# Kernel tuning notes

Measured on AMD Instinct MI355X. Metric: run time of the kernel, lower is better.

## Reference

```python
import jax, jax.numpy as jnp
import numpy as np

DIM = 64
PATCH = 8
KH = KW = 7
K = KH * KW
PAD = 3


def conv2d(x, w, pad):
    return jax.lax.conv_general_dilated(
        x, w, window_strides=(1, 1), padding=[(pad, pad), (pad, pad)],
        dimension_numbers=('NCHW', 'OIHW', 'NCHW'))


def deform_conv2d(x, offset, mask, weight):
    # torchvision modulated deformable conv v2, stride=1, dilation=1, pad=PAD
    B, C, H, W = x.shape
    off = offset.reshape(B, K, 2, H, W)  # channel pairs are (dy, dx)
    ky, kx = jnp.meshgrid(jnp.arange(KH), jnp.arange(KW), indexing='ij')
    ky = ky.reshape(K).astype(x.dtype)
    kx = kx.reshape(K).astype(x.dtype)
    hh = jnp.arange(H, dtype=x.dtype)
    ww = jnp.arange(W, dtype=x.dtype)
    # sampling locations: p0 - pad + p_k + offset, shape [B,K,H,W]
    y = hh[None, None, :, None] - PAD + ky[None, :, None, None] + off[:, :, 0]
    xx = ww[None, None, None, :] - PAD + kx[None, :, None, None] + off[:, :, 1]

    y0 = jnp.floor(y)
    x0 = jnp.floor(xx)
    wy = y - y0
    wx = xx - x0

    img_flat = x.reshape(B, C, H * W)

    def gather(yi, xi):
        valid = (yi >= 0) & (yi < H) & (xi >= 0) & (xi < W)
        yc = jnp.clip(yi, 0, H - 1).astype(jnp.int32)
        xc = jnp.clip(xi, 0, W - 1).astype(jnp.int32)
        lin = (yc * W + xc).reshape(B, -1)  # [B, K*H*W]
        v = jax.vmap(lambda im, idx: im[:, idx])(img_flat, lin)  # [B,C,K*H*W]
        v = v.reshape(B, C, K, H, W)
        return v * valid[:, None].astype(x.dtype)

    val = ((1 - wy) * (1 - wx))[:, None] * gather(y0, x0) \
        + ((1 - wy) * wx)[:, None] * gather(y0, x0 + 1) \
        + (wy * (1 - wx))[:, None] * gather(y0 + 1, x0) \
        + (wy * wx)[:, None] * gather(y0 + 1, x0 + 1)
    val = val * mask[:, None]  # modulation, [B,C,K,H,W]
    wf = weight.reshape(weight.shape[0], weight.shape[1], K)
    return jnp.einsum('bckhw,ock->bohw', val, wf)


def setup_inputs() -> dict:
    key = jax.random.key(0)
    ks = jax.random.split(key, 12)
    B, C, H, W = 1, DIM, 192, 192
    s = 0.05
    return {
        'enc': jax.random.normal(ks[0], (B, C, H, W), jnp.float32),
        'dec': jax.random.normal(ks[1], (B, C, H, W), jnp.float32),
        'inverse_offset': jax.random.normal(ks[2], (B, 2 * K, H, W), jnp.float32),
        'inverse_weight': jax.random.uniform(ks[3], (B, K, H, W), jnp.float32),
        'w_proj_in': jax.random.normal(ks[4], (C, C, 1, 1), jnp.float32) * s,
        'fft_w': 1.0 + 0.1 * jax.random.normal(ks[5], (C, 1, 1, PATCH, PATCH // 2 + 1), jnp.float32),
        'w_proj_out': jax.random.normal(ks[6], (2 * C, 2 * C, 1, 1), jnp.float32) * s,
        'w_deform': jax.random.normal(ks[7], (C, C, KH, KW), jnp.float32) * s,
        'w_conv1': jax.random.normal(ks[8], (C, C, 1, 1), jnp.float32) * s,
        'w_conv2': jax.random.normal(ks[9], (C, C, 3, 3), jnp.float32) * s,
    }


def reference(enc, dec, inverse_offset, inverse_weight, w_proj_in, fft_w,
              w_proj_out, w_deform, w_conv1, w_conv2):
    B, C, h, w = enc.shape
    reverse = deform_conv2d(enc, inverse_offset, inverse_weight, w_deform)
    reverse = conv2d(reverse, w_conv1, 0)

    e = conv2d(enc, w_proj_in, 0)
    # check_image_size: pad H,W to multiples of PATCH (no-op for 192)
    ph = (-h) % PATCH
    pw = (-w) % PATCH
    e = jnp.pad(e, ((0, 0), (0, 0), (0, ph), (0, pw)))
    Hp, Wp = h + ph, w + pw
    # [B,C,h',w',p1,p2]
    xp = e.reshape(B, C, Hp // PATCH, PATCH, Wp // PATCH, PATCH).transpose(0, 1, 2, 4, 3, 5)
    xf = jnp.fft.rfft2(xp.astype(jnp.float32)) * fft_w  # fft_w [C,1,1,8,5] broadcasts
    xp = jnp.fft.irfft2(xf, s=(PATCH, PATCH))
    e = xp.transpose(0, 1, 2, 4, 3, 5).reshape(B, C, Hp, Wp)[:, :, :h, :w]

    e = e + reverse
    e = conv2d(e, w_conv2, 1)
    feat = jnp.concatenate([e, dec], axis=1)
    feat = conv2d(feat, w_proj_out, 0)
    x1, x2 = jnp.split(feat, 2, axis=1)  # SimpleGate
    return x1 * x2
```

## Files before the change

kernel.cpp:

```cpp
#include <hip/hip_runtime.h>
#include <math.h>

#define CH    64
#define WW    192
#define HH    192
#define HWSZ  (192*192)
#define KK    49
#define ROWP  68
#define SROW  72
#define C3ROW 72
#define OROW  136

typedef __attribute__((ext_vector_type(8))) short     s16x8;
typedef __attribute__((ext_vector_type(8))) _Float16  h16x8;
typedef __attribute__((ext_vector_type(2))) _Float16  h16x2;
typedef __attribute__((ext_vector_type(2))) __fp16    fp16x2;
typedef __attribute__((ext_vector_type(4))) float     f32x4;

__device__ __forceinline__ unsigned short f2h(float f) {
    union { _Float16 h; unsigned short s; } u; u.h = (_Float16)f;
    return u.s;
}

__device__ __forceinline__ unsigned pkh(float lo, float hi) {
    union { fp16x2 h; unsigned u; } v;
    v.h = __builtin_amdgcn_cvt_pkrtz(lo, hi);
    return v.u;
}

__device__ __forceinline__ h16x2 cvt2h(float a) {
    union { fp16x2 h; h16x2 o; } v;
    v.h = __builtin_amdgcn_cvt_pkrtz(a, a);
    return v.o;
}

__device__ __forceinline__ h16x2 as_h2(unsigned u) {
    union { unsigned u; h16x2 h; } v; v.u = u; return v.h;
}

__device__ __forceinline__ unsigned as_u(h16x2 h) {
    union { h16x2 h; unsigned u; } v; v.h = h; return v.u;
}

__device__ const float c_cos8[8] = {
    1.f, 0.70710678118654752f, 0.f, -0.70710678118654752f,
   -1.f, -0.70710678118654752f, 0.f, 0.70710678118654752f };

__global__ __launch_bounds__(256) void k_prep(
    const float* __restrict__ fw,
    const float* __restrict__ wd,
    const float* __restrict__ w2,
    const float* __restrict__ wc1,
    const float* __restrict__ wpo,
    const float* __restrict__ wpi,
    float* __restrict__ krT,
    short* __restrict__ wA,
    short* __restrict__ w2A,
    short* __restrict__ wpoA,
    short* __restrict__ wpiA)
{
    int tid = blockIdx.x * blockDim.x + threadIdx.x;
    int nt  = gridDim.x * blockDim.x;
    for (int t = tid; t < 64 * 64; t += nt) {
        int uv = t >> 6, c = t & 63;
        int u = uv >> 3, v = uv & 7;
        float acc = 0.f;
        for (int ky = 0; ky < 8; ky++)
            for (int kx = 0; kx < 8; kx++) {
                float wv = (kx <= 4) ? fw[c * 40 + ky * 5 + kx]
                                     : fw[c * 40 + ((8 - ky) & 7) * 5 + (8 - kx)];
                acc += wv * c_cos8[(ky * u + kx * v) & 7];
            }
        krT[uv * 64 + c] = acc * (1.f / 64.f);
    }
    for (int t = tid; t < 9 * 4096; t += nt) {
        int tap = t / 4096, rem = t & 4095;
        int o = rem >> 6, c = rem & 63;
        float v = w2[(o * 64 + c) * 9 + tap];
        int fi = tap * 8 + (o >> 4) * 2 + (c >> 5);
        int ln = ((c >> 3) & 3) * 16 + (o & 15);
        w2A[fi * 512 + ln * 8 + (c & 7)] = (short)f2h(v);
    }
    for (int t = tid; t < 128 * 128; t += nt) {
        int o = t >> 7, c = t & 127;
        int fi = (o >> 4) * 4 + (c >> 5);
        int ln = ((c >> 3) & 3) * 16 + (o & 15);
        wpoA[fi * 512 + ln * 8 + (c & 7)] = (short)f2h(wpo[t]);
    }
    for (int t = tid; t < 64 * 64; t += nt) {
        int o = t >> 6, c = t & 63;
        int fi = (o >> 4) * 2 + (c >> 5);
        int ln = ((c >> 3) & 3) * 16 + (o & 15);
        wpiA[fi * 512 + ln * 8 + (c & 7)] = (short)f2h(wpi[t]);
    }

    __shared__ float wdk [64 * ROWP];
    __shared__ float wc1s[64 * ROWP];
    int k = blockIdx.x;
    int t = threadIdx.x;
#pragma unroll
    for (int r = 0; r < 16; r++) {
        int idx = t + r * 256;
        int o = idx >> 6, c = idx & 63;
        wdk [o * ROWP + c] = wd[(o * 64 + c) * KK + k];
        wc1s[o * ROWP + c] = wc1[o * 64 + c];
    }
    __syncthreads();

    int ot = (t >> 4) * 4, cb = (t & 15) * 4;
    float a[4][4];
#pragma unroll
    for (int i = 0; i < 4; i++)
#pragma unroll
        for (int j = 0; j < 4; j++) a[i][j] = 0.f;
    for (int o = 0; o < 64; o++) {
        float wv_[4], sv_[4];
#pragma unroll
        for (int i = 0; i < 4; i++) wv_[i] = wc1s[(ot + i) * ROWP + o];
#pragma unroll
        for (int j = 0; j < 4; j++) sv_[j] = wdk[o * ROWP + cb + j];
#pragma unroll
        for (int i = 0; i < 4; i++)
#pragma unroll
            for (int j = 0; j < 4; j++) a[i][j] += wv_[i] * sv_[j];
    }
#pragma unroll
    for (int i = 0; i < 4; i++)
#pragma unroll
        for (int j = 0; j < 4; j++) {
            int o2 = ot + i, c = cb + j;
            int tt = o2 >> 4, m = o2 & 15;
            int kt = c >> 5, q = (c >> 3) & 3, jj = c & 7;
            int ln = q * 16 + m;
            wA[(k * 8 + tt * 2 + kt) * 512 + ln * 8 + jj] = (short)f2h(a[i][j]);
        }
}

__global__ __launch_bounds__(256) void k_trans(
    const float* __restrict__ enc, unsigned short* __restrict__ encH)
{
    __shared__ float s[64 * 65];
    int t = threadIdx.x;
    int base = blockIdx.x * 64;
#pragma unroll
    for (int r = 0; r < 16; r++) {
        int idx = t + r * 256;
        int p = idx & 63, c = idx >> 6;
        s[p * 65 + c] = enc[c * HWSZ + base + p];
    }
    __syncthreads();
#pragma unroll
    for (int r = 0; r < 8; r++) {
        int idx = t + r * 256;
        int pr = idx & 31, p = idx >> 5;
        ((unsigned*)encH)[(base + p) * 32 + pr] =
            pkh(s[p * 65 + 2 * pr], s[p * 65 + 2 * pr + 1]);
    }
}

#define REDW 20

__global__ __launch_bounds__(256) void k_deform(
    const unsigned short* __restrict__ encH, const float* __restrict__ off,
    const float* __restrict__ msk, const short* __restrict__ wA,
    float* __restrict__ rev)
{
    __shared__ __align__(16) short sm[4][16 * SROW];
    __shared__ __align__(16) float red[2 * 64 * REDW];

    int t = threadIdx.x;
    int lane = t & 63, w = t >> 6;
    int b = blockIdx.x;
    int xcd = b & 7, blk = b >> 3;
    int gy  = xcd * 24 + blk / 12;
    int gx0 = (blk % 12) * 16;

    int sp = lane >> 2, g = lane & 3;
    int sgx  = gx0 + sp;
    int gp_s = gy * WW + sgx;
    int n = lane & 15, q = lane >> 4;
    short* smw = &sm[w][0];

    f32x4 acc[4];
#pragma unroll
    for (int ot = 0; ot < 4; ot++) acc[ot] = (f32x4){0.f, 0.f, 0.f, 0.f};

    int kstart = (w == 0) ? 0 : 13 + (w - 1) * 12;
    int kend   = (w == 0) ? 13 : kstart + 12;

    float dy = off[(2 * kstart) * HWSZ + gp_s];
    float dx = off[(2 * kstart + 1) * HWSZ + gp_s];
    float mm = msk[kstart * HWSZ + gp_s];

#pragma unroll 1
    for (int k = kstart; k < kend; k++) {
        int ky = k / 7, kx = k % 7;
        float y = (float)(gy  - 3 + ky) + dy;
        float x = (float)(sgx - 3 + kx) + dx;
        float y0f = floorf(y), x0f = floorf(x);
        float wy = y - y0f, wx = x - x0f;
        int iy0 = (int)y0f, ix0 = (int)x0f;
        int iy1 = iy0 + 1, ix1 = ix0 + 1;
        bool vy0 = (iy0 >= 0) & (iy0 < HH);
        bool vy1 = (iy1 >= 0) & (iy1 < HH);
        bool vx0 = (ix0 >= 0) & (ix0 < WW);
        bool vx1 = (ix1 >= 0) & (ix1 < WW);
        int iy0c = min(max(iy0, 0), HH - 1), iy1c = min(max(iy1, 0), HH - 1);
        int ix0c = min(max(ix0, 0), WW - 1), ix1c = min(max(ix1, 0), WW - 1);
        float a00 = (vy0 & vx0) ? (1.f - wy) * (1.f - wx) * mm : 0.f;
        float a01 = (vy0 & vx1) ? (1.f - wy) * wx * mm : 0.f;
        float a10 = (vy1 & vx0) ? wy * (1.f - wx) * mm : 0.f;
        float a11 = (vy1 & vx1) ? wy * wx * mm : 0.f;

        const unsigned short* b00p = encH + (iy0c * WW + ix0c) * 64 + g * 16;
        const unsigned short* b01p = encH + (iy0c * WW + ix1c) * 64 + g * 16;
        const unsigned short* b10p = encH + (iy1c * WW + ix0c) * 64 + g * 16;
        const unsigned short* b11p = encH + (iy1c * WW + ix1c) * 64 + g * 16;
        uint4 u00[2], u01[2], u10[2], u11[2];
        u00[0] = *(const uint4*)b00p;  u00[1] = *(const uint4*)(b00p + 8);
        u01[0] = *(const uint4*)b01p;  u01[1] = *(const uint4*)(b01p + 8);
        u10[0] = *(const uint4*)b10p;  u10[1] = *(const uint4*)(b10p + 8);
        u11[0] = *(const uint4*)b11p;  u11[1] = *(const uint4*)(b11p + 8);

        float dyn = 0.f, dxn = 0.f, mmn = 0.f;
        if (k + 1 < kend) {
            dyn = off[(2 * k + 2) * HWSZ + gp_s];
            dxn = off[(2 * k + 3) * HWSZ + gp_s];
            mmn = msk[(k + 1) * HWSZ + gp_s];
        }

        h16x8 af[8];
#pragma unroll
        for (int f = 0; f < 8; f++)
            af[f] = *(const h16x8*)&wA[(k * 8 + f) * 512 + lane * 8];

        h16x2 w00 = cvt2h(a00);
        h16x2 w01 = cvt2h(a01);
        h16x2 w10 = cvt2h(a10);
        h16x2 w11 = cvt2h(a11);

        unsigned c00[8] = {u00[0].x, u00[0].y, u00[0].z, u00[0].w,
                           u00[1].x, u00[1].y, u00[1].z, u00[1].w};
        unsigned c01[8] = {u01[0].x, u01[0].y, u01[0].z, u01[0].w,
                           u01[1].x, u01[1].y, u01[1].z, u01[1].w};
        unsigned c10[8] = {u10[0].x, u10[0].y, u10[0].z, u10[0].w,
                           u10[1].x, u10[1].y, u10[1].z, u10[1].w};
        unsigned c11[8] = {u11[0].x, u11[0].y, u11[0].z, u11[0].w,
                           u11[1].x, u11[1].y, u11[1].z, u11[1].w};
        unsigned pk[8];
#pragma unroll
        for (int j = 0; j < 8; j++) {
            h16x2 r = as_h2(c00[j]) * w00;
            r = as_h2(c01[j]) * w01 + r;
            r = as_h2(c10[j]) * w10 + r;
            r = as_h2(c11[j]) * w11 + r;
            pk[j] = as_u(r);
        }
        *(uint4*)&smw[sp * SROW + g * 16]     = make_uint4(pk[0], pk[1], pk[2], pk[3]);
        *(uint4*)&smw[sp * SROW + g * 16 + 8] = make_uint4(pk[4], pk[5], pk[6], pk[7]);

        h16x8 b0 = *(const h16x8*)&smw[n * SROW +  0 + q * 8];
        h16x8 b1 = *(const h16x8*)&smw[n * SROW + 32 + q * 8];

#pragma unroll
        for (int ot = 0; ot < 4; ot++) {
            acc[ot] = __builtin_amdgcn_mfma_f32_16x16x32_f16(af[ot * 2],     b0, acc[ot], 0, 0, 0);
            acc[ot] = __builtin_amdgcn_mfma_f32_16x16x32_f16(af[ot * 2 + 1], b1, acc[ot], 0, 0, 0);
        }

        dy = dyn; dx = dxn; mm = mmn;
    }

    if (w >= 2) {
        float* rp = &red[((w - 2) * 64 + lane) * REDW];
#pragma unroll
        for (int ot = 0; ot < 4; ot++)
            *(float4*)&rp[ot * 4] = make_float4(acc[ot][0], acc[ot][1], acc[ot][2], acc[ot][3]);
    }
    __syncthreads();
    if (w < 2) {
        const float* rp = &red[(w * 64 + lane) * REDW];
#pragma unroll
        for (int ot = 0; ot < 4; ot++) {
            float4 v = *(const float4*)&rp[ot * 4];
            acc[ot][0] += v.x; acc[ot][1] += v.y;
            acc[ot][2] += v.z; acc[ot][3] += v.w;
        }
    }
    __syncthreads();
    if (w == 1) {
        float* rp = &red[lane * REDW];
#pragma unroll
        for (int ot = 0; ot < 4; ot++)
            *(float4*)&rp[ot * 4] = make_float4(acc[ot][0], acc[ot][1], acc[ot][2], acc[ot][3]);
    }
    __syncthreads();
    if (w == 0) {
        const float* rp = &red[lane * REDW];
#pragma unroll
        for (int ot = 0; ot < 4; ot++) {
            float4 v = *(const float4*)&rp[ot * 4];
            acc[ot][0] += v.x; acc[ot][1] += v.y;
            acc[ot][2] += v.z; acc[ot][3] += v.w;
        }
        int gp_m = gy * WW + gx0 + n;
#pragma unroll
        for (int ot = 0; ot < 4; ot++) {
            float4 rv = make_float4(acc[ot][0], acc[ot][1], acc[ot][2], acc[ot][3]);
            *(float4*)&rev[gp_m * 64 + ot * 16 + q * 4] = rv;
        }
    }
}

__global__ __launch_bounds__(256) void k_fft(
    const unsigned short* __restrict__ encH, const short* __restrict__ wpiA,
    const float* __restrict__ krT, float* __restrict__ e1)
{
    __shared__ __align__(16) short sbf[64 * SROW];
    __shared__ __align__(16) float e0[64 * ROWP];
    int t = threadIdx.x;
    int pbx = blockIdx.x % 24, pby = blockIdx.x / 24;
    int gx0 = pbx * 8, gy0 = pby * 8;

#pragma unroll
    for (int r = 0; r < 2; r++) {
        int idx = t + r * 256;
        int px = idx >> 3, g8 = idx & 7;
        int gy = gy0 + (px >> 3), gx = gx0 + (px & 7);
        *(uint4*)&sbf[px * SROW + g8 * 8] =
            *(const uint4*)&encH[(gy * WW + gx) * 64 + g8 * 8];
    }
    __syncthreads();

    int lane = t & 63, w = t >> 6;
    int n = lane & 15, q = lane >> 4;
    h16x8 a0 = *(const h16x8*)&wpiA[(w * 2 + 0) * 512 + lane * 8];
    h16x8 a1 = *(const h16x8*)&wpiA[(w * 2 + 1) * 512 + lane * 8];
#pragma unroll
    for (int j = 0; j < 4; j++) {
        h16x8 b0 = *(const h16x8*)&sbf[(j * 16 + n) * SROW +  0 + q * 8];
        h16x8 b1 = *(const h16x8*)&sbf[(j * 16 + n) * SROW + 32 + q * 8];
        f32x4 acc = {0.f, 0.f, 0.f, 0.f};
        acc = __builtin_amdgcn_mfma_f32_16x16x32_f16(a0, b0, acc, 0, 0, 0);
        acc = __builtin_amdgcn_mfma_f32_16x16x32_f16(a1, b1, acc, 0, 0, 0);
#pragma unroll
        for (int r = 0; r < 4; r++)
            e0[(j * 16 + n) * ROWP + w * 16 + q * 4 + r] = acc[r];
    }
    __syncthreads();

    int o = t & 63;
    int yb = t >> 6;
#pragma unroll
    for (int yy = 0; yy < 2; yy++) {
        int y = yb + yy * 4;
        float outr[8];
#pragma unroll
        for (int x = 0; x < 8; x++) outr[x] = 0.f;
#pragma unroll
        for (int u = 0; u < 8; u++) {
            int ry = (y - u + 8) & 7;
            float row[8];
#pragma unroll
            for (int rx = 0; rx < 8; rx++)
                row[rx] = e0[(ry * 8 + rx) * ROWP + o];
#pragma unroll
            for (int v = 0; v < 8; v++) {
                float kv = krT[(u * 8 + v) * 64 + o];
#pragma unroll
                for (int x = 0; x < 8; x++)
                    outr[x] += kv * row[(x - v + 8) & 7];
            }
        }
        int gy = gy0 + y;
#pragma unroll
        for (int x = 0; x < 8; x++)
            e1[(gy * WW + gx0 + x) * 64 + o] = outr[x];
    }
}

__global__ __launch_bounds__(256) void k_c3out(
    const float* __restrict__ e1, const float* __restrict__ rev,
    const short* __restrict__ w2A, const float* __restrict__ dec,
    const short* __restrict__ wpoA, float* __restrict__ out)
{
    __shared__ __align__(16) short sm[4][54 * C3ROW];
    int t = threadIdx.x;
    int lane = t & 63, w = t >> 6;
    int b = blockIdx.x;
    int xcd = b & 7, blk = b >> 3;
    int gy  = xcd * 24 + blk / 3;
    int gx0 = (blk % 3) * 64 + w * 16;
    short* smw = &sm[w][0];
    int n = lane & 15, q = lane >> 4;

    for (int r = 0; r < 14; r++) {
        int u = lane + r * 64;
        if (u < 864) {
            int rp = u >> 4, g = u & 15;
            int row = rp / 18, pxl = rp - row * 18;
            int gyy = gy + row - 1, gxx = gx0 + pxl - 1;
            float4 v = make_float4(0.f, 0.f, 0.f, 0.f);
            if (gyy >= 0 && gyy < HH && gxx >= 0 && gxx < WW) {
                int gp = (gyy * WW + gxx) * 64 + g * 4;
                float4 va = *(const float4*)&e1[gp];
                float4 vb = *(const float4*)&rev[gp];
                v.x = va.x + vb.x; v.y = va.y + vb.y;
                v.z = va.z + vb.z; v.w = va.w + vb.w;
            }
            *(uint2*)&smw[rp * C3ROW + g * 4] = make_uint2(pkh(v.x, v.y), pkh(v.z, v.w));
        }
    }

    f32x4 acc[4];
#pragma unroll
    for (int ot = 0; ot < 4; ot++) acc[ot] = (f32x4){0.f, 0.f, 0.f, 0.f};

#pragma unroll 1
    for (int tap = 0; tap < 9; tap++) {
        int dy = tap / 3, dx = tap - dy * 3;
        int rp = dy * 18 + n + dx;
        h16x8 b0 = *(const h16x8*)&smw[rp * C3ROW +  0 + q * 8];
        h16x8 b1 = *(const h16x8*)&smw[rp * C3ROW + 32 + q * 8];
#pragma unroll
        for (int ot = 0; ot < 4; ot++) {
            h16x8 a0 = *(const h16x8*)&w2A[(tap * 8 + ot * 2 + 0) * 512 + lane * 8];
            h16x8 a1 = *(const h16x8*)&w2A[(tap * 8 + ot * 2 + 1) * 512 + lane * 8];
            acc[ot] = __builtin_amdgcn_mfma_f32_16x16x32_f16(a0, b0, acc[ot], 0, 0, 0);
            acc[ot] = __builtin_amdgcn_mfma_f32_16x16x32_f16(a1, b1, acc[ot], 0, 0, 0);
        }
    }

#pragma unroll
    for (int ot = 0; ot < 4; ot++) {
        unsigned lo = pkh(acc[ot][0], acc[ot][1]);
        unsigned hi = pkh(acc[ot][2], acc[ot][3]);
        *(uint2*)&smw[n * OROW + ot * 16 + q * 4] = make_uint2(lo, hi);
    }
    {
        int gp = gy * WW + gx0 + n;
        unsigned pk[8];
#pragma unroll
        for (int i = 0; i < 8; i++) {
            float va = dec[(q * 16 + 2 * i)     * HWSZ + gp];
            float vb = dec[(q * 16 + 2 * i + 1) * HWSZ + gp];
            pk[i] = pkh(va, vb);
        }
        *(uint4*)&smw[n * OROW + 64 + q * 16]     = make_uint4(pk[0], pk[1], pk[2], pk[3]);
        *(uint4*)&smw[n * OROW + 64 + q * 16 + 8] = make_uint4(pk[4], pk[5], pk[6], pk[7]);
    }

    f32x4 go[8];
#pragma unroll
    for (int ot = 0; ot < 8; ot++) go[ot] = (f32x4){0.f, 0.f, 0.f, 0.f};

#pragma unroll 1
    for (int kt = 0; kt < 4; kt++) {
        h16x8 bb = *(const h16x8*)&smw[n * OROW + kt * 32 + q * 8];
#pragma unroll
        for (int ot = 0; ot < 8; ot++) {
            h16x8 aa = *(const h16x8*)&wpoA[(ot * 4 + kt) * 512 + lane * 8];
            go[ot] = __builtin_amdgcn_mfma_f32_16x16x32_f16(aa, bb, go[ot], 0, 0, 0);
        }
    }

    int gp = gy * WW + gx0 + n;
#pragma unroll
    for (int ot = 0; ot < 4; ot++)
#pragma unroll
        for (int r = 0; r < 4; r++)
            out[(ot * 16 + q * 4 + r) * HWSZ + gp] = go[ot][r] * go[ot + 4][r];
}

extern "C" void kernel_launch(void* const* d_in, const int* in_sizes, int n_in,
                              void* d_out, int out_size, void* d_ws, size_t ws_size,
                              hipStream_t stream)
{
    const float* enc  = (const float*)d_in[0];
    const float* dec  = (const float*)d_in[1];
    const float* ioff = (const float*)d_in[2];
    const float* iwt  = (const float*)d_in[3];
    const float* wpi  = (const float*)d_in[4];
    const float* fw   = (const float*)d_in[5];
    const float* wpo  = (const float*)d_in[6];
    const float* wd   = (const float*)d_in[7];
    const float* wc1  = (const float*)d_in[8];
    const float* wc2  = (const float*)d_in[9];
    float* out = (float*)d_out;
    float* ws  = (float*)d_ws;

    float*          krT  = ws;
    float*          rev  = ws + 4096;
    float*          e1   = ws + 2363392;
    unsigned short* encH = (unsigned short*)(ws + 4722688);
    short*          wA   = (short*)(ws + 5902336);
    short*          w2A  = (short*)(ws + 6002688);
    short*          wpoA = (short*)(ws + 6021120);
    short*          wpiA = (short*)(ws + 6029312);

    hipLaunchKernelGGL(k_prep,   dim3(49),   dim3(256), 0, stream,
                       fw, wd, wc2, wc1, wpo, wpi, krT, wA, w2A, wpoA, wpiA);
    hipLaunchKernelGGL(k_trans,  dim3(576),  dim3(256), 0, stream, enc, encH);
    hipLaunchKernelGGL(k_deform, dim3(2304), dim3(256), 0, stream, encH, ioff, iwt, wA, rev);
    hipLaunchKernelGGL(k_fft,    dim3(576),  dim3(256), 0, stream, encH, wpiA, krT, e1);
    hipLaunchKernelGGL(k_c3out,  dim3(576),  dim3(256), 0, stream, e1, rev, w2A, dec, wpoA, out);
}
```

Baseline: 214.1 us.

## Merge independent kernels into shared launches and store intermediates in fp16

Folds the weight-prep and enc transpose into one launch, and the deformable conv and FFT branch into another, with block-index ranges selecting the role. The intermediate rev and e1 tensors and the FFT's shared-memory stage are now stored as fp16, halving their traffic. In k_c3out the e1+rev sum is done in fp16. The aim is to cut launch overhead and tail idle time, and to reduce memory bandwidth. The cost is some precision loss in the intermediates.

```diff
diff --git a/kernel.cpp b/kernel.cpp
--- a/kernel.cpp
+++ b/kernel.cpp
@@ -22,6 +22,11 @@
     return u.s;
 }
 
+__device__ __forceinline__ float h2f(unsigned short s) {
+    union { unsigned short s; _Float16 h; } u; u.s = s;
+    return (float)u.h;
+}
+
 __device__ __forceinline__ unsigned pkh(float lo, float hi) {
     union { fp16x2 h; unsigned u; } v;
     v.h = __builtin_amdgcn_cvt_pkrtz(lo, hi);
@@ -46,7 +51,9 @@
     1.f, 0.70710678118654752f, 0.f, -0.70710678118654752f,
    -1.f, -0.70710678118654752f, 0.f, 0.70710678118654752f };
 
-__global__ __launch_bounds__(256) void k_prep(
+__global__ __launch_bounds__(256) void k_pt(
+    const float* __restrict__ enc,
+    unsigned short* __restrict__ encH,
     const float* __restrict__ fw,
     const float* __restrict__ wd,
     const float* __restrict__ w2,
@@ -59,50 +66,73 @@
     short* __restrict__ wpoA,
     short* __restrict__ wpiA)
 {
-    int tid = blockIdx.x * blockDim.x + threadIdx.x;
-    int nt  = gridDim.x * blockDim.x;
-    for (int t = tid; t < 64 * 64; t += nt) {
-        int uv = t >> 6, c = t & 63;
-        int u = uv >> 3, v = uv & 7;
+    __shared__ __align__(16) char smem_raw[2 * 64 * ROWP * 4];
+    int b = blockIdx.x;
+    int t = threadIdx.x;
+
+    if (b < 576) {
+        float* s = (float*)smem_raw;
+        int base = b * 64;
+#pragma unroll
+        for (int r = 0; r < 16; r++) {
+            int idx = t + r * 256;
+            int p = idx & 63, c = idx >> 6;
+            s[p * 65 + c] = enc[c * HWSZ + base + p];
+        }
+        __syncthreads();
+#pragma unroll
+        for (int r = 0; r < 8; r++) {
+            int idx = t + r * 256;
+            int pr = idx & 31, p = idx >> 5;
+            ((unsigned*)encH)[(base + p) * 32 + pr] =
+                pkh(s[p * 65 + 2 * pr], s[p * 65 + 2 * pr + 1]);
+        }
+        return;
+    }
+
+    int kb = b - 576;
+    int tid = kb * 256 + t;
+    int nt  = 49 * 256;
+    for (int u = tid; u < 64 * 64; u += nt) {
+        int uv = u >> 6, c = u & 63;
+        int uu = uv >> 3, v = uv & 7;
         float acc = 0.f;
         for (int ky = 0; ky < 8; ky++)
             for (int kx = 0; kx < 8; kx++) {
                 float wv = (kx <= 4) ? fw[c * 40 + ky * 5 + kx]
                                      : fw[c * 40 + ((8 - ky) & 7) * 5 + (8 - kx)];
-                acc += wv * c_cos8[(ky * u + kx * v) & 7];
+                acc += wv * c_cos8[(ky * uu + kx * v) & 7];
             }
         krT[uv * 64 + c] = acc * (1.f / 64.f);
     }
-    for (int t = tid; t < 9 * 4096; t += nt) {
-        int tap = t / 4096, rem = t & 4095;
+    for (int u = tid; u < 9 * 4096; u += nt) {
+        int tap = u / 4096, rem = u & 4095;
         int o = rem >> 6, c = rem & 63;
         float v = w2[(o * 64 + c) * 9 + tap];
         int fi = tap * 8 + (o >> 4) * 2 + (c >> 5);
         int ln = ((c >> 3) & 3) * 16 + (o & 15);
         w2A[fi * 512 + ln * 8 + (c & 7)] = (short)f2h(v);
     }
-    for (int t = tid; t < 128 * 128; t += nt) {
-        int o = t >> 7, c = t & 127;
+    for (int u = tid; u < 128 * 128; u += nt) {
+        int o = u >> 7, c = u & 127;
         int fi = (o >> 4) * 4 + (c >> 5);
         int ln = ((c >> 3) & 3) * 16 + (o & 15);
-        wpoA[fi * 512 + ln * 8 + (c & 7)] = (short)f2h(wpo[t]);
-    }
-    for (int t = tid; t < 64 * 64; t += nt) {
-        int o = t >> 6, c = t & 63;
+        wpoA[fi * 512 + ln * 8 + (c & 7)] = (short)f2h(wpo[u]);
+    }
+    for (int u = tid; u < 64 * 64; u += nt) {
+        int o = u >> 6, c = u & 63;
         int fi = (o >> 4) * 2 + (c >> 5);
         int ln = ((c >> 3) & 3) * 16 + (o & 15);
-        wpiA[fi * 512 + ln * 8 + (c & 7)] = (short)f2h(wpi[t]);
-    }
-
-    __shared__ float wdk [64 * ROWP];
-    __shared__ float wc1s[64 * ROWP];
-    int k = blockIdx.x;
-    int t = threadIdx.x;
+        wpiA[fi * 512 + ln * 8 + (c & 7)] = (short)f2h(wpi[u]);
+    }
+
+    float* wdk  = (float*)smem_raw;
+    float* wc1s = wdk + 64 * ROWP;
 #pragma unroll
     for (int r = 0; r < 16; r++) {
         int idx = t + r * 256;
         int o = idx >> 6, c = idx & 63;
-        wdk [o * ROWP + c] = wd[(o * 64 + c) * KK + k];
+        wdk [o * ROWP + c] = wd[(o * 64 + c) * KK + kb];
         wc1s[o * ROWP + c] = wc1[o * 64 + c];
     }
     __syncthreads();
@@ -132,255 +162,239 @@
             int tt = o2 >> 4, m = o2 & 15;
             int kt = c >> 5, q = (c >> 3) & 3, jj = c & 7;
             int ln = q * 16 + m;
-            wA[(k * 8 + tt * 2 + kt) * 512 + ln * 8 + jj] = (short)f2h(a[i][j]);
-        }
-}
-
-__global__ __launch_bounds__(256) void k_trans(
-    const float* __restrict__ enc, unsigned short* __restrict__ encH)
-{
-    __shared__ float s[64 * 65];
-    int t = threadIdx.x;
-    int base = blockIdx.x * 64;
-#pragma unroll
-    for (int r = 0; r < 16; r++) {
-        int idx = t + r * 256;
-        int p = idx & 63, c = idx >> 6;
-        s[p * 65 + c] = enc[c * HWSZ + base + p];
-    }
-    __syncthreads();
-#pragma unroll
-    for (int r = 0; r < 8; r++) {
-        int idx = t + r * 256;
-        int pr = idx & 31, p = idx >> 5;
-        ((unsigned*)encH)[(base + p) * 32 + pr] =
-            pkh(s[p * 65 + 2 * pr], s[p * 65 + 2 * pr + 1]);
-    }
+            wA[(kb * 8 + tt * 2 + kt) * 512 + ln * 8 + jj] = (short)f2h(a[i][j]);
+        }
 }
 
 #define REDW 20
 
-__global__ __launch_bounds__(256) void k_deform(
+__global__ __launch_bounds__(256) void k_dff(
     const unsigned short* __restrict__ encH, const float* __restrict__ off,
     const float* __restrict__ msk, const short* __restrict__ wA,
-    float* __restrict__ rev)
+    unsigned short* __restrict__ revH,
+    const short* __restrict__ wpiA, const float* __restrict__ krT,
+    unsigned short* __restrict__ e1H)
 {
-    __shared__ __align__(16) short sm[4][16 * SROW];
-    __shared__ __align__(16) float red[2 * 64 * REDW];
-
+    __shared__ __align__(16) char smem_raw[19456];
     int t = threadIdx.x;
     int lane = t & 63, w = t >> 6;
     int b = blockIdx.x;
-    int xcd = b & 7, blk = b >> 3;
-    int gy  = xcd * 24 + blk / 12;
-    int gx0 = (blk % 12) * 16;
-
-    int sp = lane >> 2, g = lane & 3;
-    int sgx  = gx0 + sp;
-    int gp_s = gy * WW + sgx;
-    int n = lane & 15, q = lane >> 4;
-    short* smw = &sm[w][0];
-
-    f32x4 acc[4];
-#pragma unroll
-    for (int ot = 0; ot < 4; ot++) acc[ot] = (f32x4){0.f, 0.f, 0.f, 0.f};
-
-    int kstart = (w == 0) ? 0 : 13 + (w - 1) * 12;
-    int kend   = (w == 0) ? 13 : kstart + 12;
-
-    float dy = off[(2 * kstart) * HWSZ + gp_s];
-    float dx = off[(2 * kstart + 1) * HWSZ + gp_s];
-    float mm = msk[kstart * HWSZ + gp_s];
+
+    if (b < 2304) {
+        short* sm_base = (short*)smem_raw;
+        float* red = (float*)(smem_raw + 4 * 16 * SROW * 2);
+
+        int xcd = b & 7, blk = b >> 3;
+        int gy  = xcd * 24 + blk / 12;
+        int gx0 = (blk % 12) * 16;
+
+        int sp = lane >> 2, g = lane & 3;
+        int sgx  = gx0 + sp;
+        int gp_s = gy * WW + sgx;
+        int n = lane & 15, q = lane >> 4;
+        short* smw = sm_base + w * (16 * SROW);
+
+        f32x4 acc[4];
+#pragma unroll
+        for (int ot = 0; ot < 4; ot++) acc[ot] = (f32x4){0.f, 0.f, 0.f, 0.f};
+
+        int kstart = (w == 0) ? 0 : 13 + (w - 1) * 12;
+        int kend   = (w == 0) ? 13 : kstart + 12;
+
+        float dy = off[(2 * kstart) * HWSZ + gp_s];
+        float dx = off[(2 * kstart + 1) * HWSZ + gp_s];
+        float mm = msk[kstart * HWSZ + gp_s];
 
 #pragma unroll 1
-    for (int k = kstart; k < kend; k++) {
-        int ky = k / 7, kx = k % 7;
-        float y = (float)(gy  - 3 + ky) + dy;
-        float x = (float)(sgx - 3 + kx) + dx;
-        float y0f = floorf(y), x0f = floorf(x);
-        float wy = y - y0f, wx = x - x0f;
-        int iy0 = (int)y0f, ix0 = (int)x0f;
-        int iy1 = iy0 + 1, ix1 = ix0 + 1;
-        bool vy0 = (iy0 >= 0) & (iy0 < HH);
-        bool vy1 = (iy1 >= 0) & (iy1 < HH);
-        bool vx0 = (ix0 >= 0) & (ix0 < WW);
-        bool vx1 = (ix1 >= 0) & (ix1 < WW);
-        int iy0c = min(max(iy0, 0), HH - 1), iy1c = min(max(iy1, 0), HH - 1);
-        int ix0c = min(max(ix0, 0), WW - 1), ix1c = min(max(ix1, 0), WW - 1);
-        float a00 = (vy0 & vx0) ? (1.f - wy) * (1.f - wx) * mm : 0.f;
-        float a01 = (vy0 & vx1) ? (1.f - wy) * wx * mm : 0.f;
-        float a10 = (vy1 & vx0) ? wy * (1.f - wx) * mm : 0.f;
-        float a11 = (vy1 & vx1) ? wy * wx * mm : 0.f;
-
-        const unsigned short* b00p = encH + (iy0c * WW + ix0c) * 64 + g * 16;
-        const unsigned short* b01p = encH + (iy0c * WW + ix1c) * 64 + g * 16;
-        const unsigned short* b10p = encH + (iy1c * WW + ix0c) * 64 + g * 16;
-        const unsigned short* b11p = encH + (iy1c * WW + ix1c) * 64 + g * 16;
-        uint4 u00[2], u01[2], u10[2], u11[2];
-        u00[0] = *(const uint4*)b00p;  u00[1] = *(const uint4*)(b00p + 8);
-        u01[0] = *(const uint4*)b01p;  u01[1] = *(const uint4*)(b01p + 8);
-        u10[0] = *(const uint4*)b10p;  u10[1] = *(const uint4*)(b10p + 8);
-        u11[0] = *(const uint4*)b11p;  u11[1] = *(const uint4*)(b11p + 8);
-
-        float dyn = 0.f, dxn = 0.f, mmn = 0.f;
-        if (k + 1 < kend) {
-            dyn = off[(2 * k + 2) * HWSZ + gp_s];
-            dxn = off[(2 * k + 3) * HWSZ + gp_s];
-            mmn = msk[(k + 1) * HWSZ + gp_s];
-        }
-
-        h16x8 af[8];
-#pragma unroll
-        for (int f = 0; f < 8; f++)
-            af[f] = *(const h16x8*)&wA[(k * 8 + f) * 512 + lane * 8];
-
-        h16x2 w00 = cvt2h(a00);
-        h16x2 w01 = cvt2h(a01);
-        h16x2 w10 = cvt2h(a10);
-        h16x2 w11 = cvt2h(a11);
-
-        unsigned c00[8] = {u00[0].x, u00[0].y, u00[0].z, u00[0].w,
-                           u00[1].x, u00[1].y, u00[1].z, u00[1].w};
-        unsigned c01[8] = {u01[0].x, u01[0].y, u01[0].z, u01[0].w,
-                           u01[1].x, u01[1].y, u01[1].z, u01[1].w};
-        unsigned c10[8] = {u10[0].x, u10[0].y, u10[0].z, u10[0].w,
-                           u10[1].x, u10[1].y, u10[1].z, u10[1].w};
-        unsigned c11[8] = {u11[0].x, u11[0].y, u11[0].z, u11[0].w,
-                           u11[1].x, u11[1].y, u11[1].z, u11[1].w};
-        unsigned pk[8];
-#pragma unroll
-        for (int j = 0; j < 8; j++) {
-            h16x2 r = as_h2(c00[j]) * w00;
-            r = as_h2(c01[j]) * w01 + r;
-            r = as_h2(c10[j]) * w10 + r;
-            r = as_h2(c11[j]) * w11 + r;
-            pk[j] = as_u(r);
-        }
-        *(uint4*)&smw[sp * SROW + g * 16]     = make_uint4(pk[0], pk[1], pk[2], pk[3]);
-        *(uint4*)&smw[sp * SROW + g * 16 + 8] = make_uint4(pk[4], pk[5], pk[6], pk[7]);
-
-        h16x8 b0 = *(const h16x8*)&smw[n * SROW +  0 + q * 8];
-        h16x8 b1 = *(const h16x8*)&smw[n * SROW + 32 + q * 8];
-
-#pragma unroll
-        for (int ot = 0; ot < 4; ot++) {
-            acc[ot] = __builtin_amdgcn_mfma_f32_16x16x32_f16(af[ot * 2],     b0, acc[ot], 0, 0, 0);
-            acc[ot] = __builtin_amdgcn_mfma_f32_16x16x32_f16(af[ot * 2 + 1], b1, acc[ot], 0, 0, 0);
-        }
-
-        dy = dyn; dx = dxn; mm = mmn;
-    }
-
-    if (w >= 2) {
-        float* rp = &red[((w - 2) * 64 + lane) * REDW];
-#pragma unroll
-        for (int ot = 0; ot < 4; ot++)
-            *(float4*)&rp[ot * 4] = make_float4(acc[ot][0], acc[ot][1], acc[ot][2], acc[ot][3]);
-    }
-    __syncthreads();
-    if (w < 2) {
-        const float* rp = &red[(w * 64 + lane) * REDW];
-#pragma unroll
-        for (int ot = 0; ot < 4; ot++) {
-            float4 v = *(const float4*)&rp[ot * 4];
-            acc[ot][0] += v.x; acc[ot][1] += v.y;
-            acc[ot][2] += v.z; acc[ot][3] += v.w;
-        }
-    }
-    __syncthreads();
-    if (w == 1) {
-        float* rp = &red[lane * REDW];
-#pragma unroll
-        for (int ot = 0; ot < 4; ot++)
-            *(float4*)&rp[ot * 4] = make_float4(acc[ot][0], acc[ot][1], acc[ot][2], acc[ot][3]);
-    }
-    __syncthreads();
-    if (w == 0) {
-        const float* rp = &red[lane * REDW];
-#pragma unroll
-        for (int ot = 0; ot < 4; ot++) {
-            float4 v = *(const float4*)&rp[ot * 4];
-            acc[ot][0] += v.x; acc[ot][1] += v.y;
-            acc[ot][2] += v.z; acc[ot][3] += v.w;
-        }
-        int gp_m = gy * WW + gx0 + n;
-#pragma unroll
-        for (int ot = 0; ot < 4; ot++) {
-            float4 rv = make_float4(acc[ot][0], acc[ot][1], acc[ot][2], acc[ot][3]);
-            *(float4*)&rev[gp_m * 64 + ot * 16 + q * 4] = rv;
-        }
-    }
-}
-
-__global__ __launch_bounds__(256) void k_fft(
-    const unsigned short* __restrict__ encH, const short* __restrict__ wpiA,
-    const float* __restrict__ krT, float* __restrict__ e1)
-{
-    __shared__ __align__(16) short sbf[64 * SROW];
-    __shared__ __align__(16) float e0[64 * ROWP];
-    int t = threadIdx.x;
-    int pbx = blockIdx.x % 24, pby = blockIdx.x / 24;
-    int gx0 = pbx * 8, gy0 = pby * 8;
-
-#pragma unroll
-    for (int r = 0; r < 2; r++) {
-        int idx = t + r * 256;
-        int px = idx >> 3, g8 = idx & 7;
-        int gy = gy0 + (px >> 3), gx = gx0 + (px & 7);
-        *(uint4*)&sbf[px * SROW + g8 * 8] =
-            *(const uint4*)&encH[(gy * WW + gx) * 64 + g8 * 8];
-    }
-    __syncthreads();
-
-    int lane = t & 63, w = t >> 6;
-    int n = lane & 15, q = lane >> 4;
-    h16x8 a0 = *(const h16x8*)&wpiA[(w * 2 + 0) * 512 + lane * 8];
-    h16x8 a1 = *(const h16x8*)&wpiA[(w * 2 + 1) * 512 + lane * 8];
-#pragma unroll
-    for (int j = 0; j < 4; j++) {
-        h16x8 b0 = *(const h16x8*)&sbf[(j * 16 + n) * SROW +  0 + q * 8];
-        h16x8 b1 = *(const h16x8*)&sbf[(j * 16 + n) * SROW + 32 + q * 8];
-        f32x4 acc = {0.f, 0.f, 0.f, 0.f};
-        acc = __builtin_amdgcn_mfma_f32_16x16x32_f16(a0, b0, acc, 0, 0, 0);
-        acc = __builtin_amdgcn_mfma_f32_16x16x32_f16(a1, b1, acc, 0, 0, 0);
-#pragma unroll
-        for (int r = 0; r < 4; r++)
-            e0[(j * 16 + n) * ROWP + w * 16 + q * 4 + r] = acc[r];
-    }
-    __syncthreads();
-
-    int o = t & 63;
-    int yb = t >> 6;
-#pragma unroll
-    for (int yy = 0; yy < 2; yy++) {
-        int y = yb + yy * 4;
-        float outr[8];
-#pragma unroll
-        for (int x = 0; x < 8; x++) outr[x] = 0.f;
-#pragma unroll
-        for (int u = 0; u < 8; u++) {
-            int ry = (y - u + 8) & 7;
-            float row[8];
-#pragma unroll
-            for (int rx = 0; rx < 8; rx++)
-                row[rx] = e0[(ry * 8 + rx) * ROWP + o];
-#pragma unroll
-            for (int v = 0; v < 8; v++) {
-                float kv = krT[(u * 8 + v) * 64 + o];
-#pragma unroll
-                for (int x = 0; x < 8; x++)
-                    outr[x] += kv * row[(x - v + 8) & 7];
-            }
-        }
-        int gy = gy0 + y;
-#pragma unroll
-        for (int x = 0; x < 8; x++)
-            e1[(gy * WW + gx0 + x) * 64 + o] = outr[x];
+        for (int k = kstart; k < kend; k++) {
+            int ky = k / 7, kx = k % 7;
+            float y = (float)(gy  - 3 + ky) + dy;
+            float x = (float)(sgx - 3 + kx) + dx;
+            float y0f = floorf(y), x0f = floorf(x);
+            float wy = y - y0f, wx = x - x0f;
+            int iy0 = (int)y0f, ix0 = (int)x0f;
+            int iy1 = iy0 + 1, ix1 = ix0 + 1;
+            bool vy0 = (iy0 >= 0) & (iy0 < HH);
+            bool vy1 = (iy1 >= 0) & (iy1 < HH);
+            bool vx0 = (ix0 >= 0) & (ix0 < WW);
+            bool vx1 = (ix1 >= 0) & (ix1 < WW);
+            int iy0c = min(max(iy0, 0), HH - 1), iy1c = min(max(iy1, 0), HH - 1);
+            int ix0c = min(max(ix0, 0), WW - 1), ix1c = min(max(ix1, 0), WW - 1);
+            float a00 = (vy0 & vx0) ? (1.f - wy) * (1.f - wx) * mm : 0.f;
+            float a01 = (vy0 & vx1) ? (1.f - wy) * wx * mm : 0.f;
+            float a10 = (vy1 & vx0) ? wy * (1.f - wx) * mm : 0.f;
+            float a11 = (vy1 & vx1) ? wy * wx * mm : 0.f;
+
+            const unsigned short* b00p = encH + (iy0c * WW + ix0c) * 64 + g * 16;
+            const unsigned short* b01p = encH + (iy0c * WW + ix1c) * 64 + g * 16;
+            const unsigned short* b10p = encH + (iy1c * WW + ix0c) * 64 + g * 16;
+            const unsigned short* b11p = encH + (iy1c * WW + ix1c) * 64 + g * 16;
+            uint4 u00[2], u01[2], u10[2], u11[2];
+            u00[0] = *(const uint4*)b00p;  u00[1] = *(const uint4*)(b00p + 8);
+            u01[0] = *(const uint4*)b01p;  u01[1] = *(const uint4*)(b01p + 8);
+            u10[0] = *(const uint4*)b10p;  u10[1] = *(const uint4*)(b10p + 8);
+            u11[0] = *(const uint4*)b11p;  u11[1] = *(const uint4*)(b11p + 8);
+
+            float dyn = 0.f, dxn = 0.f, mmn = 0.f;
+            if (k + 1 < kend) {
+                dyn = off[(2 * k + 2) * HWSZ + gp_s];
+                dxn = off[(2 * k + 3) * HWSZ + gp_s];
+                mmn = msk[(k + 1) * HWSZ + gp_s];
+            }
+
+            h16x8 af[8];
+#pragma unroll
+            for (int f = 0; f < 8; f++)
+                af[f] = *(const h16x8*)&wA[(k * 8 + f) * 512 + lane * 8];
+
+            h16x2 w00 = cvt2h(a00);
+            h16x2 w01 = cvt2h(a01);
+            h16x2 w10 = cvt2h(a10);
+            h16x2 w11 = cvt2h(a11);
+
+            unsigned c00[8] = {u00[0].x, u00[0].y, u00[0].z, u00[0].w,
+                               u00[1].x, u00[1].y, u00[1].z, u00[1].w};
+            unsigned c01[8] = {u01[0].x, u01[0].y, u01[0].z, u01[0].w,
+                               u01[1].x, u01[1].y, u01[1].z, u01[1].w};
+            unsigned c10[8] = {u10[0].x, u10[0].y, u10[0].z, u10[0].w,
+                               u10[1].x, u10[1].y, u10[1].z, u10[1].w};
+            unsigned c11[8] = {u11[0].x, u11[0].y, u11[0].z, u11[0].w,
+                               u11[1].x, u11[1].y, u11[1].z, u11[1].w};
+            unsigned pk[8];
+#pragma unroll
+            for (int j = 0; j < 8; j++) {
+                h16x2 r = as_h2(c00[j]) * w00;
+                r = as_h2(c01[j]) * w01 + r;
+                r = as_h2(c10[j]) * w10 + r;
+                r = as_h2(c11[j]) * w11 + r;
+                pk[j] = as_u(r);
+            }
+            *(uint4*)&smw[sp * SROW + g * 16]     = make_uint4(pk[0], pk[1], pk[2], pk[3]);
+            *(uint4*)&smw[sp * SROW + g * 16 + 8] = make_uint4(pk[4], pk[5], pk[6], pk[7]);
+
+            h16x8 b0 = *(const h16x8*)&smw[n * SROW +  0 + q * 8];
+            h16x8 b1 = *(const h16x8*)&smw[n * SROW + 32 + q * 8];
+
+#pragma unroll
+            for (int ot = 0; ot < 4; ot++) {
+                acc[ot] = __builtin_amdgcn_mfma_f32_16x16x32_f16(af[ot * 2],     b0, acc[ot], 0, 0, 0);
+                acc[ot] = __builtin_amdgcn_mfma_f32_16x16x32_f16(af[ot * 2 + 1], b1, acc[ot], 0, 0, 0);
+            }
+
+            dy = dyn; dx = dxn; mm = mmn;
+        }
+
+        if (w >= 2) {
+            float* rp = &red[((w - 2) * 64 + lane) * REDW];
+#pragma unroll
+            for (int ot = 0; ot < 4; ot++)
+                *(float4*)&rp[ot * 4] = make_float4(acc[ot][0], acc[ot][1], acc[ot][2], acc[ot][3]);
+        }
+        __syncthreads();
+        if (w < 2) {
+            const float* rp = &red[(w * 64 + lane) * REDW];
+#pragma unroll
+            for (int ot = 0; ot < 4; ot++) {
+                float4 v = *(const float4*)&rp[ot * 4];
+                acc[ot][0] += v.x; acc[ot][1] += v.y;
+                acc[ot][2] += v.z; acc[ot][3] += v.w;
+            }
+        }
+        __syncthreads();
+        if (w == 1) {
+            float* rp = &red[lane * REDW];
+#pragma unroll
+            for (int ot = 0; ot < 4; ot++)
+                *(float4*)&rp[ot * 4] = make_float4(acc[ot][0], acc[ot][1], acc[ot][2], acc[ot][3]);
+        }
+        __syncthreads();
+        if (w == 0) {
+            const float* rp = &red[lane * REDW];
+#pragma unroll
+            for (int ot = 0; ot < 4; ot++) {
+                float4 v = *(const float4*)&rp[ot * 4];
+                acc[ot][0] += v.x; acc[ot][1] += v.y;
+                acc[ot][2] += v.z; acc[ot][3] += v.w;
+            }
+            int gp_m = gy * WW + gx0 + n;
+#pragma unroll
+            for (int ot = 0; ot < 4; ot++) {
+                unsigned u0 = pkh(acc[ot][0], acc[ot][1]);
+                unsigned u1 = pkh(acc[ot][2], acc[ot][3]);
+                *(uint2*)&revH[gp_m * 64 + ot * 16 + q * 4] = make_uint2(u0, u1);
+            }
+        }
+        return;
+    }
+
+    {
+        short* sbf = (short*)smem_raw;
+        short* e0H = (short*)(smem_raw + 64 * SROW * 2);
+
+        int pb = b - 2304;
+        int pbx = pb % 24, pby = pb / 24;
+        int gx0 = pbx * 8, gy0 = pby * 8;
+
+#pragma unroll
+        for (int r = 0; r < 2; r++) {
+            int idx = t + r * 256;
+            int px = idx >> 3, g8 = idx & 7;
+            int gy = gy0 + (px >> 3), gx = gx0 + (px & 7);
+            *(uint4*)&sbf[px * SROW + g8 * 8] =
+                *(const uint4*)&encH[(gy * WW + gx) * 64 + g8 * 8];
+        }
+        __syncthreads();
+
+        int n = lane & 15, q = lane >> 4;
+        h16x8 a0 = *(const h16x8*)&wpiA[(w * 2 + 0) * 512 + lane * 8];
+        h16x8 a1 = *(const h16x8*)&wpiA[(w * 2 + 1) * 512 + lane * 8];
+#pragma unroll
+        for (int j = 0; j < 4; j++) {
+            h16x8 b0 = *(const h16x8*)&sbf[(j * 16 + n) * SROW +  0 + q * 8];
+            h16x8 b1 = *(const h16x8*)&sbf[(j * 16 + n) * SROW + 32 + q * 8];
+            f32x4 acc = {0.f, 0.f, 0.f, 0.f};
+            acc = __builtin_amdgcn_mfma_f32_16x16x32_f16(a0, b0, acc, 0, 0, 0);
+            acc = __builtin_amdgcn_mfma_f32_16x16x32_f16(a1, b1, acc, 0, 0, 0);
+            unsigned u0 = pkh(acc[0], acc[1]);
+            unsigned u1 = pkh(acc[2], acc[3]);
+            *(unsigned*)&e0H[(j * 16 + n) * SROW + w * 16 + q * 4]     = u0;
+            *(unsigned*)&e0H[(j * 16 + n) * SROW + w * 16 + q * 4 + 2] = u1;
+        }
+        __syncthreads();
+
+        int o = t & 63;
+        int yb = t >> 6;
+#pragma unroll
+        for (int yy = 0; yy < 2; yy++) {
+            int y = yb + yy * 4;
+            float outr[8];
+#pragma unroll
+            for (int x = 0; x < 8; x++) outr[x] = 0.f;
+#pragma unroll
+            for (int u = 0; u < 8; u++) {
+                int ry = (y - u + 8) & 7;
+                float row[8];
+#pragma unroll
+                for (int rx = 0; rx < 8; rx++)
+                    row[rx] = h2f(((const unsigned short*)e0H)[(ry * 8 + rx) * SROW + o]);
+#pragma unroll
+                for (int v = 0; v < 8; v++) {
+                    float kv = krT[(u * 8 + v) * 64 + o];
+#pragma unroll
+                    for (int x = 0; x < 8; x++)
+                        outr[x] += kv * row[(x - v + 8) & 7];
+                }
+            }
+            int gy = gy0 + y;
+#pragma unroll
+            for (int x = 0; x < 8; x++)
+                e1H[(gy * WW + gx0 + x) * 64 + o] = f2h(outr[x]);
+        }
     }
 }
 
 __global__ __launch_bounds__(256) void k_c3out(
-    const float* __restrict__ e1, const float* __restrict__ rev,
+    const unsigned short* __restrict__ e1H, const unsigned short* __restrict__ revH,
     const short* __restrict__ w2A, const float* __restrict__ dec,
     const short* __restrict__ wpoA, float* __restrict__ out)
 {
@@ -400,15 +414,15 @@
             int rp = u >> 4, g = u & 15;
             int row = rp / 18, pxl = rp - row * 18;
             int gyy = gy + row - 1, gxx = gx0 + pxl - 1;
-            float4 v = make_float4(0.f, 0.f, 0.f, 0.f);
+            uint2 v = make_uint2(0u, 0u);
             if (gyy >= 0 && gyy < HH && gxx >= 0 && gxx < WW) {
                 int gp = (gyy * WW + gxx) * 64 + g * 4;
-                float4 va = *(const float4*)&e1[gp];
-                float4 vb = *(const float4*)&rev[gp];
-                v.x = va.x + vb.x; v.y = va.y + vb.y;
-                v.z = va.z + vb.z; v.w = va.w + vb.w;
-            }
-            *(uint2*)&smw[rp * C3ROW + g * 4] = make_uint2(pkh(v.x, v.y), pkh(v.z, v.w));
+                uint2 va = *(const uint2*)&e1H[gp];
+                uint2 vb = *(const uint2*)&revH[gp];
+                v.x = as_u(as_h2(va.x) + as_h2(vb.x));
+                v.y = as_u(as_h2(va.y) + as_h2(vb.y));
+            }
+            *(uint2*)&smw[rp * C3ROW + g * 4] = v;
         }
     }
 
@@ -490,18 +504,18 @@
     float* ws  = (float*)d_ws;
 
     float*          krT  = ws;
-    float*          rev  = ws + 4096;
-    float*          e1   = ws + 2363392;
-    unsigned short* encH = (unsigned short*)(ws + 4722688);
-    short*          wA   = (short*)(ws + 5902336);
-    short*          w2A  = (short*)(ws + 6002688);
-    short*          wpoA = (short*)(ws + 6021120);
-    short*          wpiA = (short*)(ws + 6029312);
-
-    hipLaunchKernelGGL(k_prep,   dim3(49),   dim3(256), 0, stream,
-                       fw, wd, wc2, wc1, wpo, wpi, krT, wA, w2A, wpoA, wpiA);
-    hipLaunchKernelGGL(k_trans,  dim3(576),  dim3(256), 0, stream, enc, encH);
-    hipLaunchKernelGGL(k_deform, dim3(2304), dim3(256), 0, stream, encH, ioff, iwt, wA, rev);
-    hipLaunchKernelGGL(k_fft,    dim3(576),  dim3(256), 0, stream, encH, wpiA, krT, e1);
-    hipLaunchKernelGGL(k_c3out,  dim3(576),  dim3(256), 0, stream, e1, rev, w2A, dec, wpoA, out);
-}
+    unsigned short* revH = (unsigned short*)(ws + 4096);
+    unsigned short* e1H  = (unsigned short*)(ws + 1183744);
+    unsigned short* encH = (unsigned short*)(ws + 2363392);
+    short*          wA   = (short*)(ws + 3543040);
+    short*          w2A  = (short*)(ws + 3643392);
+    short*          wpoA = (short*)(ws + 3661824);
+    short*          wpiA = (short*)(ws + 3670016);
+
+    hipLaunchKernelGGL(k_pt,    dim3(625),  dim3(256), 0, stream,
+                       enc, encH, fw, wd, wc2, wc1, wpo, wpi, krT, wA, w2A, wpoA, wpiA);
+    hipLaunchKernelGGL(k_dff,   dim3(2880), dim3(256), 0, stream,
+                       encH, ioff, iwt, wA, revH, wpiA, krT, e1H);
+    hipLaunchKernelGGL(k_c3out, dim3(576),  dim3(256), 0, stream,
+                       e1H, revH, w2A, dec, wpoA, out);
+}
```

After: 189.8 us. 1.13x faster.
